# Performance work log

Measured on AMD Instinct MI355X. Metric: run time of the kernel, lower is better.

Reference implementation:

```python
import jax, jax.numpy as jnp
import numpy as np

B, T, N = 32, 720, 321
K = 25        # moving-average kernel_size (init kwarg)
DEC_LEV = 3   # wavelet decomposition level (init kwarg)
F = 16        # sym8 filter length
A = 0.85      # soft-threshold shrink factor from the source

# pywt sym8 decomposition low-pass filter
_DEC_LO = np.array([
    -0.0033824159510061256, -0.00054213233179114812, 0.031695087811492981,
    0.0076074873249176054, -0.14329423835080971, -0.061273359067658524,
    0.48135965125837221, 0.77718575170052351, 0.36444189483533893,
    -0.051945838107709037, -0.027219029917056003, 0.049137179673607506,
    0.0038087520138906151, -0.014952258337048231, -0.0003029205147213668,
    0.0018899503327594609], dtype=np.float32)
_DEC_HI = (((-1.0) ** (np.arange(F) + 1)) * _DEC_LO[::-1]).astype(np.float32)
DEC_LO = jnp.asarray(_DEC_LO)
DEC_HI = jnp.asarray(_DEC_HI)
REC_LO = DEC_LO[::-1]
REC_HI = DEC_HI[::-1]


def _dwt(a):
    # single-level DWT, pywt 'symmetric' extension, downsample odd phase
    ext = jnp.pad(a, (F - 1, F - 1), mode='symmetric')
    ca = jnp.convolve(ext, DEC_LO, mode='valid')[1::2]
    cd = jnp.convolve(ext, DEC_HI, mode='valid')[1::2]
    return ca, cd


def _idwt(ca, cd):
    # upsample (zeros in odd slots), full conv with reconstruction filters, trim F-2
    L = ca.shape[0]
    up_a = jnp.zeros(2 * L - 1, ca.dtype).at[::2].set(ca)
    up_d = jnp.zeros(2 * L - 1, cd.dtype).at[::2].set(cd)
    rec = jnp.convolve(up_a, REC_LO) + jnp.convolve(up_d, REC_HI)
    return rec[F - 2: rec.shape[0] - (F - 2)]


def _denoise(sig):
    # wavedec -> universal soft-threshold (shrunk by A) on all detail levels -> waverec
    L = sig.shape[0]
    a = sig
    details = []  # details[0] = finest level cD1
    for _ in range(DEC_LEV):
        a, d = _dwt(a)
        details.append(d)
    sigma = jnp.median(jnp.abs(details[0])) / 0.6745
    lam = sigma * jnp.sqrt(jnp.float32(2.0 * np.log(float(L))))
    details = [jnp.where(jnp.abs(d) >= lam,
                         jnp.sign(d) * (jnp.abs(d) - A * lam),
                         jnp.zeros_like(d)) for d in details]
    for d in reversed(details):
        if a.shape[0] == d.shape[0] + 1:  # static-shape pywt length fixup
            a = a[:-1]
        a = _idwt(a, d)
    return a


def _moving_avg(x):
    # replicate-pad (K-1)//2 on both ends of time axis, then AvgPool1d(K, stride=1)
    p = (K - 1) // 2
    xp = jnp.concatenate([jnp.repeat(x[:, :1], p, axis=1), x,
                          jnp.repeat(x[:, -1:], p, axis=1)], axis=1)
    s = jax.lax.reduce_window(xp, 0.0, jax.lax.add, (1, K, 1), (1, 1, 1), 'VALID')
    return s / K


def _forward(x):
    trend = _moving_avg(x)            # [B,T,N]
    res = x - trend
    # T is even so the odd-length branch of the original is never taken
    trend_nn = _denoise(trend.reshape(-1)).reshape(x.shape)
    res_nn = _denoise(res.reshape(-1)).reshape(x.shape)
    return trend - trend_nn, trend_nn, res - res_nn, res_nn


def setup_inputs() -> dict:
    key = jax.random.key(0)
    return {"x": jax.random.normal(key, (B, T, N), dtype=jnp.float32)}


def reference(x):
    return _forward(x)
```

## Files before the change

### kernel.cpp

```cpp
#include <hip/hip_runtime.h>
#include <math.h>

#define BB 32
#define TT 720
#define NNN 321
#define KK 25
#define PP 12
#define TCH 48

constexpr int L0 = BB * TT * NNN;
constexpr int L1 = (L0 + 15) / 2;
constexpr int L2 = (L1 + 15) / 2;
constexpr int L3 = (L2 + 15) / 2;
constexpr unsigned KMED = (unsigned)((L1 - 1) / 2 + 1);
constexpr float AA = 0.85f;

constexpr float DLO[16] = {
    -0.0033824159510061256f, -0.0005421323317911481f, 0.03169508781149298f,
    0.007607487324917605f,  -0.1432942383508097f,    -0.061273359067658524f,
    0.4813596512583722f,     0.7771857517005235f,     0.36444189483533895f,
    -0.05194583810770904f,  -0.027219029917056003f,   0.049137179673607506f,
    0.003808752013890615f,  -0.01495225833704823f,   -0.0003029205147213668f,
    0.0018899503327594609f };

__global__ void mavg_kernel(const float* __restrict__ x,
                            float* __restrict__ trend,
                            float* __restrict__ res) {
    constexpr int NCH = TT / TCH;
    int gid = blockIdx.x * blockDim.x + threadIdx.x;
    if (gid >= BB * NCH * NNN) return;
    int n    = gid % NNN;
    int rest = gid / NNN;
    int ch   = rest % NCH;
    int b    = rest / NCH;
    int t0   = ch * TCH;
    const float* xb = x + (size_t)b * TT * NNN + n;
    float sum = 0.f;
#pragma unroll
    for (int dt = -PP; dt <= PP; ++dt) {
        int tt = t0 + dt;
        tt = tt < 0 ? 0 : (tt >= TT ? TT - 1 : tt);
        sum += xb[(size_t)tt * NNN];
    }
    size_t base = (size_t)b * TT * NNN + (size_t)t0 * NNN + n;
    for (int i = 0; i < TCH; ++i) {
        int t = t0 + i;
        float tr = sum * (1.0f / (float)KK);
        size_t idx = base + (size_t)i * NNN;
        trend[idx] = tr;
        res[idx] = xb[(size_t)t * NNN] - tr;
        int tp = t + 1 + PP; if (tp > TT - 1) tp = TT - 1;
        int tm = t - PP;     if (tm < 0)      tm = 0;
        sum += xb[(size_t)tp * NNN] - xb[(size_t)tm * NNN];
    }
}

__global__ void dwt_kernel(const float* __restrict__ in0,
                           const float* __restrict__ in1,
                           int Lin, int Lout,
                           float* __restrict__ ca, float* __restrict__ cd) {
    int o0 = (blockIdx.x * blockDim.x + threadIdx.x) * 2;
    int s = blockIdx.y;
    if (o0 >= Lout) return;
    const float* a = s ? in1 : in0;
    if (2 * o0 - 14 >= 0 && 2 * o0 + 3 < Lin && o0 + 1 < Lout) {
        const float* p = a + 2 * o0 - 14;
        float v[18];
#pragma unroll
        for (int j = 0; j < 18; ++j) v[j] = p[j];
        float slo0 = 0.f, shi0 = 0.f, slo1 = 0.f, shi1 = 0.f;
#pragma unroll
        for (int j = 0; j < 16; ++j) {
            float h = (j & 1) ? DLO[15 - j] : -DLO[15 - j];
            slo0 = fmaf(DLO[j], v[15 - j], slo0);
            shi0 = fmaf(h,      v[15 - j], shi0);
            slo1 = fmaf(DLO[j], v[17 - j], slo1);
            shi1 = fmaf(h,      v[17 - j], shi1);
        }
        ca[(size_t)s * Lout + o0]     = slo0;
        cd[(size_t)s * Lout + o0]     = shi0;
        ca[(size_t)s * Lout + o0 + 1] = slo1;
        cd[(size_t)s * Lout + o0 + 1] = shi1;
    } else {
        int oend = (o0 + 2 < Lout) ? o0 + 2 : Lout;
        for (int o = o0; o < oend; ++o) {
            float slo = 0.f, shi = 0.f;
            int bidx = 2 * o + 1;
#pragma unroll
            for (int j = 0; j < 16; ++j) {
                int idx = bidx - j;
                if (idx < 0) idx = -1 - idx;
                if (idx >= Lin) idx = 2 * Lin - 1 - idx;
                float v = a[idx];
                slo = fmaf(DLO[j], v, slo);
                float h = (j & 1) ? DLO[15 - j] : -DLO[15 - j];
                shi = fmaf(h, v, shi);
            }
            ca[(size_t)s * Lout + o] = slo;
            cd[(size_t)s * Lout + o] = shi;
        }
    }
}

__device__ __forceinline__ float sthr(float d, float lam, float alam) {
    float ad = fabsf(d);
    return (ad >= lam) ? copysignf(ad - alam, d) : 0.f;
}

__device__ __forceinline__ void idwt_pair(const float* __restrict__ ca,
                                          const float* __restrict__ cd,
                                          int q, float lam, float alam,
                                          float& v0, float& v1) {
    float a0 = 0.f, a1 = 0.f;
#pragma unroll
    for (int p = 0; p < 8; ++p) {
        float a = ca[q + p];
        float d = sthr(cd[q + p], lam, alam);
        a0 = fmaf(a, DLO[2 * p + 1], a0);
        a0 = fmaf(d, DLO[14 - 2 * p], a0);
        a1 = fmaf(a, DLO[2 * p], a1);
        a1 = fmaf(d, -DLO[15 - 2 * p], a1);
    }
    v0 = a0; v1 = a1;
}

__global__ void idwt_mid(const float* __restrict__ coefA,
                         const float* __restrict__ coefD,
                         int Lc, int M,
                         float* __restrict__ out,
                         const float* __restrict__ lamArr) {
    int q = blockIdx.x * blockDim.x + threadIdx.x;
    int s = blockIdx.y;
    int r0 = 2 * q;
    if (r0 >= M) return;
    float lam = lamArr[s];
    float alam = AA * lam;
    const float* ca = coefA + (size_t)s * Lc;
    const float* cd = coefD + (size_t)s * Lc;
    float v0, v1;
    idwt_pair(ca, cd, q, lam, alam, v0, v1);
    float* o = out + (size_t)s * M;
    o[r0] = v0;
    if (r0 + 1 < M) o[r0 + 1] = v1;
}

__global__ void idwt_final(const float* __restrict__ coefA,
                           const float* __restrict__ coefD,
                           const float* __restrict__ trend,
                           const float* __restrict__ res,
                           float* __restrict__ out,
                           const float* __restrict__ lamArr) {
    int q = blockIdx.x * blockDim.x + threadIdx.x;
    int s = blockIdx.y;
    int r0 = 2 * q;
    if (r0 >= L0) return;
    float lam = lamArr[s];
    float alam = AA * lam;
    const float* ca = coefA + (size_t)s * L1;
    const float* cd = coefD + (size_t)s * L1;
    float v0, v1;
    idwt_pair(ca, cd, q, lam, alam, v0, v1);
    const float* orig = s ? res : trend;
    float* o_diff = out + (size_t)(2 * s) * L0;
    float* o_nn   = out + (size_t)(2 * s + 1) * L0;
    int r1 = r0 + 1;
    o_nn[r0] = v0;  o_diff[r0] = orig[r0] - v0;
    o_nn[r1] = v1;  o_diff[r1] = orig[r1] - v1;
}

__global__ void init_median(unsigned* __restrict__ hist,
                            unsigned* __restrict__ prefix,
                            unsigned* __restrict__ kArr) {
    int t = blockIdx.x * blockDim.x + threadIdx.x;
    if (t < 8192) hist[t] = 0;
    if (t < 2) { prefix[t] = 0; kArr[t] = KMED; }
}

__global__ void hist_kernel(const float* __restrict__ d,
                            unsigned* __restrict__ hist,
                            const unsigned* __restrict__ prefix,
                            int pass) {
    int s = blockIdx.y;
    const float* ds = d + (size_t)s * L1;
    __shared__ unsigned sh[4096];
    for (int b = threadIdx.x; b < 4096; b += 256) sh[b] = 0;
    __syncthreads();
    unsigned pref = pass ? prefix[s] : 0u;
    int stride = gridDim.x * blockDim.x;
    for (int i = blockIdx.x * blockDim.x + threadIdx.x; i < L1; i += stride) {
        unsigned u = __float_as_uint(fabsf(ds[i]));
        if (pass == 0) {
            atomicAdd(&sh[u >> 20], 1u);
        } else if (pass == 1) {
            if ((u >> 20) == (pref >> 20)) atomicAdd(&sh[(u >> 8) & 0xFFFu], 1u);
        } else {
            if ((u >> 8) == (pref >> 8)) atomicAdd(&sh[u & 0xFFu], 1u);
        }
    }
    __syncthreads();
    for (int b = threadIdx.x; b < 4096; b += 256) {
        unsigned c = sh[b];
        if (c) atomicAdd(&hist[s * 4096 + b], c);
    }
}

__global__ void select_kernel(unsigned* __restrict__ hist,
                              unsigned* __restrict__ prefix,
                              unsigned* __restrict__ kArr,
                              float* __restrict__ lamArr,
                              int nbins, int shift) {
    int s = blockIdx.x;
    int t = threadIdx.x;
    __shared__ unsigned sc[256];
    __shared__ unsigned base_s;
    if (t == 0) base_s = 0;
    __syncthreads();
    unsigned k = kArr[s];
    for (int c0 = 0; c0 < nbins; c0 += 256) {
        unsigned c = hist[s * 4096 + c0 + t];
        hist[s * 4096 + c0 + t] = 0;
        sc[t] = c;
        __syncthreads();
        for (int off = 1; off < 256; off <<= 1) {
            unsigned v = (t >= off) ? sc[t - off] : 0u;
            __syncthreads();
            sc[t] += v;
            __syncthreads();
        }
        unsigned incl = base_s + sc[t];
        unsigned excl = incl - c;
        if (excl < k && incl >= k) {
            unsigned npref = prefix[s] | ((unsigned)(c0 + t) << shift);
            prefix[s] = npref;
            kArr[s] = k - excl;
            if (shift == 0) {
                float med = __uint_as_float(npref);
                float sigma = med / 0.6745f;
                lamArr[s] = sigma * sqrtf(2.0f * logf((float)L0));
            }
        }
        __syncthreads();
        if (t == 255) base_s += sc[255];
        __syncthreads();
    }
}

extern "C" void kernel_launch(void* const* d_in, const int* in_sizes, int n_in,
                              void* d_out, int out_size, void* d_ws, size_t ws_size,
                              hipStream_t stream) {
    const float* x = (const float*)d_in[0];
    float* out = (float*)d_out;
    float* w = (float*)d_ws;

    float* trend = w;
    float* res   = w + (size_t)L0;
    float* ca1   = w + 2 * (size_t)L0;
    float* cd1   = ca1 + 2 * (size_t)L1;
    float* ca2   = cd1 + 2 * (size_t)L1;
    float* cd2   = ca2 + 2 * (size_t)L2;
    float* ca3   = cd2 + 2 * (size_t)L2;
    float* cd3   = ca3 + 2 * (size_t)L3;
    float* fend  = cd3 + 2 * (size_t)L3;
    unsigned* hist   = (unsigned*)ca2;
    unsigned* prefix = (unsigned*)fend;
    unsigned* kArr   = prefix + 2;
    float*    lamArr = (float*)(kArr + 2);

    dim3 b256(256);

    init_median<<<32, b256, 0, stream>>>(hist, prefix, kArr);
    {
        int nthreads = BB * (TT / TCH) * NNN;
        mavg_kernel<<<(nthreads + 255) / 256, b256, 0, stream>>>(x, trend, res);
    }
    dwt_kernel<<<dim3(((L1 + 1) / 2 + 255) / 256, 2), b256, 0, stream>>>(trend, res, L0, L1, ca1, cd1);

    hist_kernel<<<dim3(512, 2), b256, 0, stream>>>(cd1, hist, prefix, 0);
    select_kernel<<<2, b256, 0, stream>>>(hist, prefix, kArr, lamArr, 4096, 20);
    hist_kernel<<<dim3(512, 2), b256, 0, stream>>>(cd1, hist, prefix, 1);
    select_kernel<<<2, b256, 0, stream>>>(hist, prefix, kArr, lamArr, 4096, 8);
    hist_kernel<<<dim3(512, 2), b256, 0, stream>>>(cd1, hist, prefix, 2);
    select_kernel<<<2, b256, 0, stream>>>(hist, prefix, kArr, lamArr, 256, 0);

    dwt_kernel<<<dim3(((L2 + 1) / 2 + 255) / 256, 2), b256, 0, stream>>>(ca1, ca1 + L1, L1, L2, ca2, cd2);
    dwt_kernel<<<dim3(((L3 + 1) / 2 + 255) / 256, 2), b256, 0, stream>>>(ca2, ca2 + L2, L2, L3, ca3, cd3);

    idwt_mid<<<dim3(((L2 + 1) / 2 + 255) / 256, 2), b256, 0, stream>>>(ca3, cd3, L3, L2, ca2, lamArr);
    idwt_mid<<<dim3(((L1 + 1) / 2 + 255) / 256, 2), b256, 0, stream>>>(ca2, cd2, L2, L1, ca1, lamArr);
    idwt_final<<<dim3((L0 / 2 + 255) / 256, 2), b256, 0, stream>>>(ca1, cd1, trend, res, out, lamArr);
}
```

Measured before the change: 363.3 us.

## Fuse DWT levels 2-3 and all IDWT levels into shared-memory tiled kernels

Level-2 and level-3 DWT now run in one kernel that stages ca1 tiles in LDS and keeps ca2 on-chip. The three inverse DWT passes are merged into one kernel that rebuilds levels 2 and 1 in shared memory from halo-extended tiles and writes the outputs with float2 stores. Together these remove the global round trips of ca2 and the intermediate reconstructions. The select kernel switches to a wave-shuffle scan over per-thread chunks, and the moving-average time chunk is halved. The cost is redundant halo computation and more LDS use per block.

```diff
diff --git a/kernel.cpp b/kernel.cpp
--- a/kernel.cpp
+++ b/kernel.cpp
@@ -6,7 +6,7 @@
 #define NNN 321
 #define KK 25
 #define PP 12
-#define TCH 48
+#define TCH 24
 
 constexpr int L0 = BB * TT * NNN;
 constexpr int L1 = (L0 + 15) / 2;
@@ -14,6 +14,14 @@
 constexpr int L3 = (L2 + 15) / 2;
 constexpr unsigned KMED = (unsigned)((L1 - 1) / 2 + 1);
 constexpr float AA = 0.85f;
+
+#define NC3 1024
+constexpr int LEN2T = 2 * NC3 + 32;
+constexpr int LEN1T = 4 * NC3 + 80;
+#define NF0 4096
+constexpr int N1T = NF0 / 2 + 8;
+constexpr int N2T = N1T / 2 + 7;
+constexpr int NQ3 = (N2T + 1) / 2;
 
 constexpr float DLO[16] = {
     -0.0033824159510061256f, -0.0005421323317911481f, 0.03169508781149298f,
@@ -102,70 +110,145 @@
     }
 }
 
+__global__ void dwt23_kernel(const float* __restrict__ ca1,
+                             float* __restrict__ cd2,
+                             float* __restrict__ ca3,
+                             float* __restrict__ cd3) {
+    int s = blockIdx.y;
+    int C0 = blockIdx.x * NC3;
+    const float* a1 = ca1 + (size_t)s * L1;
+    __shared__ float s1[LEN1T];
+    __shared__ float s2[LEN2T];
+    int T0 = 2 * C0 - 14;
+    int S1 = 4 * C0 - 42; if (S1 < 0) S1 = 0;
+    int E1 = 2 * (T0 + LEN2T) + 2; if (E1 > L1) E1 = L1;
+    int len1 = E1 - S1;
+    for (int i = threadIdx.x; i < len1; i += 256) s1[i] = a1[S1 + i];
+    __syncthreads();
+    float* pcd2 = cd2 + (size_t)s * L2;
+    for (int i = threadIdx.x; i < LEN2T; i += 256) {
+        int e = T0 + i;
+        if (e < 0 || e >= L2) continue;
+        int base = 2 * e + 1;
+        float slo = 0.f, shi = 0.f;
+#pragma unroll
+        for (int j = 0; j < 16; ++j) {
+            int idx = base - j;
+            if (idx < 0) idx = -1 - idx;
+            if (idx >= L1) idx = 2 * L1 - 1 - idx;
+            float v = s1[idx - S1];
+            slo = fmaf(DLO[j], v, slo);
+            float h = (j & 1) ? DLO[15 - j] : -DLO[15 - j];
+            shi = fmaf(h, v, shi);
+        }
+        s2[i] = slo;
+        if (e >= 2 * C0 && e < 2 * C0 + 2 * NC3) pcd2[e] = shi;
+    }
+    __syncthreads();
+    for (int i = threadIdx.x; i < LEN2T; i += 256) {
+        int e = T0 + i;
+        if (e < 0)        s2[i] = s2[(-1 - e) - T0];
+        else if (e >= L2) s2[i] = s2[(2 * L2 - 1 - e) - T0];
+    }
+    __syncthreads();
+    float* pca3 = ca3 + (size_t)s * L3;
+    float* pcd3 = cd3 + (size_t)s * L3;
+    for (int i = threadIdx.x; i < NC3; i += 256) {
+        int o = C0 + i;
+        if (o >= L3) break;
+        int b2 = 2 * o + 1 - T0;
+        float slo = 0.f, shi = 0.f;
+#pragma unroll
+        for (int j = 0; j < 16; ++j) {
+            float v = s2[b2 - j];
+            slo = fmaf(DLO[j], v, slo);
+            float h = (j & 1) ? DLO[15 - j] : -DLO[15 - j];
+            shi = fmaf(h, v, shi);
+        }
+        pca3[o] = slo;
+        pcd3[o] = shi;
+    }
+}
+
 __device__ __forceinline__ float sthr(float d, float lam, float alam) {
     float ad = fabsf(d);
     return (ad >= lam) ? copysignf(ad - alam, d) : 0.f;
 }
 
-__device__ __forceinline__ void idwt_pair(const float* __restrict__ ca,
-                                          const float* __restrict__ cd,
-                                          int q, float lam, float alam,
-                                          float& v0, float& v1) {
-    float a0 = 0.f, a1 = 0.f;
-#pragma unroll
-    for (int p = 0; p < 8; ++p) {
-        float a = ca[q + p];
-        float d = sthr(cd[q + p], lam, alam);
-        a0 = fmaf(a, DLO[2 * p + 1], a0);
-        a0 = fmaf(d, DLO[14 - 2 * p], a0);
-        a1 = fmaf(a, DLO[2 * p], a1);
-        a1 = fmaf(d, -DLO[15 - 2 * p], a1);
-    }
-    v0 = a0; v1 = a1;
-}
-
-__global__ void idwt_mid(const float* __restrict__ coefA,
-                         const float* __restrict__ coefD,
-                         int Lc, int M,
-                         float* __restrict__ out,
-                         const float* __restrict__ lamArr) {
-    int q = blockIdx.x * blockDim.x + threadIdx.x;
-    int s = blockIdx.y;
-    int r0 = 2 * q;
-    if (r0 >= M) return;
-    float lam = lamArr[s];
-    float alam = AA * lam;
-    const float* ca = coefA + (size_t)s * Lc;
-    const float* cd = coefD + (size_t)s * Lc;
-    float v0, v1;
-    idwt_pair(ca, cd, q, lam, alam, v0, v1);
-    float* o = out + (size_t)s * M;
-    o[r0] = v0;
-    if (r0 + 1 < M) o[r0 + 1] = v1;
-}
-
-__global__ void idwt_final(const float* __restrict__ coefA,
-                           const float* __restrict__ coefD,
+__global__ void idwt_fused(const float* __restrict__ ca3,
+                           const float* __restrict__ cd3,
+                           const float* __restrict__ cd2,
+                           const float* __restrict__ cd1,
                            const float* __restrict__ trend,
                            const float* __restrict__ res,
                            float* __restrict__ out,
                            const float* __restrict__ lamArr) {
-    int q = blockIdx.x * blockDim.x + threadIdx.x;
     int s = blockIdx.y;
-    int r0 = 2 * q;
-    if (r0 >= L0) return;
-    float lam = lamArr[s];
-    float alam = AA * lam;
-    const float* ca = coefA + (size_t)s * L1;
-    const float* cd = coefD + (size_t)s * L1;
-    float v0, v1;
-    idwt_pair(ca, cd, q, lam, alam, v0, v1);
+    int F0 = blockIdx.x * NF0;
+    float lam = lamArr[s], alam = AA * lam;
+    const float* pa3 = ca3 + (size_t)s * L3;
+    const float* pd3 = cd3 + (size_t)s * L3;
+    const float* pd2 = cd2 + (size_t)s * L2;
+    const float* pd1 = cd1 + (size_t)s * L1;
+    __shared__ float r2[N2T + 1];
+    __shared__ float r1[N1T];
+    int A1 = F0 >> 1, A2 = F0 >> 2, Q3 = F0 >> 3;
+    for (int i = threadIdx.x; i < NQ3; i += 256) {
+        int q3 = Q3 + i;
+        float a0 = 0.f, a1 = 0.f;
+#pragma unroll
+        for (int p = 0; p < 8; ++p) {
+            int idx = q3 + p; if (idx > L3 - 1) idx = L3 - 1;
+            float a = pa3[idx];
+            float d = sthr(pd3[idx], lam, alam);
+            a0 = fmaf(a, DLO[2 * p + 1], a0);
+            a0 = fmaf(d, DLO[14 - 2 * p], a0);
+            a1 = fmaf(a, DLO[2 * p], a1);
+            a1 = fmaf(d, -DLO[15 - 2 * p], a1);
+        }
+        r2[2 * i] = a0; r2[2 * i + 1] = a1;
+    }
+    __syncthreads();
+    for (int i = threadIdx.x; i < N1T / 2; i += 256) {
+        int q2 = A2 + i;
+        float a0 = 0.f, a1 = 0.f;
+#pragma unroll
+        for (int p = 0; p < 8; ++p) {
+            float a = r2[i + p];
+            int idx = q2 + p; if (idx > L2 - 1) idx = L2 - 1;
+            float d = sthr(pd2[idx], lam, alam);
+            a0 = fmaf(a, DLO[2 * p + 1], a0);
+            a0 = fmaf(d, DLO[14 - 2 * p], a0);
+            a1 = fmaf(a, DLO[2 * p], a1);
+            a1 = fmaf(d, -DLO[15 - 2 * p], a1);
+        }
+        r1[2 * i] = a0; r1[2 * i + 1] = a1;
+    }
+    __syncthreads();
     const float* orig = s ? res : trend;
     float* o_diff = out + (size_t)(2 * s) * L0;
     float* o_nn   = out + (size_t)(2 * s + 1) * L0;
-    int r1 = r0 + 1;
-    o_nn[r0] = v0;  o_diff[r0] = orig[r0] - v0;
-    o_nn[r1] = v1;  o_diff[r1] = orig[r1] - v1;
+    for (int i = threadIdx.x; i < NF0 / 2; i += 256) {
+        int q1 = A1 + i;
+        int r0 = 2 * q1;
+        if (r0 >= L0) break;
+        float a0 = 0.f, a1 = 0.f;
+#pragma unroll
+        for (int p = 0; p < 8; ++p) {
+            float a = r1[i + p];
+            int idx = q1 + p; if (idx > L1 - 1) idx = L1 - 1;
+            float d = sthr(pd1[idx], lam, alam);
+            a0 = fmaf(a, DLO[2 * p + 1], a0);
+            a0 = fmaf(d, DLO[14 - 2 * p], a0);
+            a1 = fmaf(a, DLO[2 * p], a1);
+            a1 = fmaf(d, -DLO[15 - 2 * p], a1);
+        }
+        float o0 = orig[r0], o1 = orig[r0 + 1];
+        float2 nn; nn.x = a0; nn.y = a1;
+        float2 df; df.x = o0 - a0; df.y = o1 - a1;
+        *(float2*)(o_nn + r0)   = nn;
+        *(float2*)(o_diff + r0) = df;
+    }
 }
 
 __global__ void init_median(unsigned* __restrict__ hist,
@@ -209,39 +292,42 @@
                               unsigned* __restrict__ kArr,
                               float* __restrict__ lamArr,
                               int nbins, int shift) {
-    int s = blockIdx.x;
-    int t = threadIdx.x;
-    __shared__ unsigned sc[256];
-    __shared__ unsigned base_s;
-    if (t == 0) base_s = 0;
-    __syncthreads();
+    int s = blockIdx.x, t = threadIdx.x;
+    int chunk = nbins >> 8;
+    unsigned loc[16];
+    unsigned* hs = hist + s * 4096 + t * chunk;
+    unsigned csum = 0;
+    for (int j = 0; j < chunk; ++j) { loc[j] = hs[j]; hs[j] = 0; csum += loc[j]; }
+    unsigned v = csum;
+    int lane = t & 63, wv = t >> 6;
+#pragma unroll
+    for (int off = 1; off < 64; off <<= 1) {
+        unsigned u = (unsigned)__shfl_up((int)v, off, 64);
+        if (lane >= off) v += u;
+    }
+    __shared__ unsigned wsum[4];
+    if (lane == 63) wsum[wv] = v;
+    __syncthreads();
+    unsigned base = 0;
+    for (int w2 = 0; w2 < wv; ++w2) base += wsum[w2];
+    unsigned incl = base + v, excl = incl - csum;
     unsigned k = kArr[s];
-    for (int c0 = 0; c0 < nbins; c0 += 256) {
-        unsigned c = hist[s * 4096 + c0 + t];
-        hist[s * 4096 + c0 + t] = 0;
-        sc[t] = c;
-        __syncthreads();
-        for (int off = 1; off < 256; off <<= 1) {
-            unsigned v = (t >= off) ? sc[t - off] : 0u;
-            __syncthreads();
-            sc[t] += v;
-            __syncthreads();
-        }
-        unsigned incl = base_s + sc[t];
-        unsigned excl = incl - c;
-        if (excl < k && incl >= k) {
-            unsigned npref = prefix[s] | ((unsigned)(c0 + t) << shift);
-            prefix[s] = npref;
-            kArr[s] = k - excl;
-            if (shift == 0) {
-                float med = __uint_as_float(npref);
-                float sigma = med / 0.6745f;
-                lamArr[s] = sigma * sqrtf(2.0f * logf((float)L0));
+    if (excl < k && incl >= k) {
+        unsigned run = excl;
+        for (int j = 0; j < chunk; ++j) {
+            if (run < k && run + loc[j] >= k) {
+                unsigned digit = (unsigned)(t * chunk + j);
+                unsigned npref = prefix[s] | (digit << shift);
+                prefix[s] = npref;
+                kArr[s] = k - run;
+                if (shift == 0) {
+                    float med = __uint_as_float(npref);
+                    lamArr[s] = (med / 0.6745f) * sqrtf(2.0f * logf((float)L0));
+                }
+                break;
             }
-        }
-        __syncthreads();
-        if (t == 255) base_s += sc[255];
-        __syncthreads();
+            run += loc[j];
+        }
     }
 }
 
@@ -256,13 +342,11 @@
     float* res   = w + (size_t)L0;
     float* ca1   = w + 2 * (size_t)L0;
     float* cd1   = ca1 + 2 * (size_t)L1;
-    float* ca2   = cd1 + 2 * (size_t)L1;
-    float* cd2   = ca2 + 2 * (size_t)L2;
+    float* cd2   = cd1 + 2 * (size_t)L1;
     float* ca3   = cd2 + 2 * (size_t)L2;
     float* cd3   = ca3 + 2 * (size_t)L3;
-    float* fend  = cd3 + 2 * (size_t)L3;
-    unsigned* hist   = (unsigned*)ca2;
-    unsigned* prefix = (unsigned*)fend;
+    unsigned* hist   = (unsigned*)(cd3 + 2 * (size_t)L3);
+    unsigned* prefix = hist + 8192;
     unsigned* kArr   = prefix + 2;
     float*    lamArr = (float*)(kArr + 2);
 
@@ -282,10 +366,8 @@
     hist_kernel<<<dim3(512, 2), b256, 0, stream>>>(cd1, hist, prefix, 2);
     select_kernel<<<2, b256, 0, stream>>>(hist, prefix, kArr, lamArr, 256, 0);
 
-    dwt_kernel<<<dim3(((L2 + 1) / 2 + 255) / 256, 2), b256, 0, stream>>>(ca1, ca1 + L1, L1, L2, ca2, cd2);
-    dwt_kernel<<<dim3(((L3 + 1) / 2 + 255) / 256, 2), b256, 0, stream>>>(ca2, ca2 + L2, L2, L3, ca3, cd3);
-
-    idwt_mid<<<dim3(((L2 + 1) / 2 + 255) / 256, 2), b256, 0, stream>>>(ca3, cd3, L3, L2, ca2, lamArr);
-    idwt_mid<<<dim3(((L1 + 1) / 2 + 255) / 256, 2), b256, 0, stream>>>(ca2, cd2, L2, L1, ca1, lamArr);
-    idwt_final<<<dim3((L0 / 2 + 255) / 256, 2), b256, 0, stream>>>(ca1, cd1, trend, res, out, lamArr);
-}
+    dwt23_kernel<<<dim3((L3 + NC3 - 1) / NC3, 2), b256, 0, stream>>>(ca1, cd2, ca3, cd3);
+
+    idwt_fused<<<dim3((L0 + NF0 - 1) / NF0, 2), b256, 0, stream>>>(
+        ca3, cd3, cd2, cd1, trend, res, out, lamArr);
+}
```

Measured after the change: 334.2 us. 1.09x faster.
